# Optimization experiments

Hardware: AMD Instinct MI355X
Metric: run time of the kernel (lower is better)

The kernel has to match this reference:

```python
import jax, jax.numpy as jnp
import numpy as np

N = 50000
IN_CH = 64
HID_CH = 32
NEG_SLOPE = 0.2  # PyG GATConv default for attention LeakyReLU


def _glorot(key, shape):
    fan = shape[0] + shape[-1] if len(shape) > 1 else shape[0]
    s = jnp.sqrt(6.0 / fan)
    return jax.random.uniform(key, shape, jnp.float32, -s, s)


def setup_inputs() -> dict:
    key = jax.random.key(0)
    ks = jax.random.split(key, 20)
    x = jax.random.normal(ks[0], (N, IN_CH), jnp.float32)
    edge_index = jax.random.randint(ks[1], (2, 800000), 0, N, jnp.int64)
    dims = [(IN_CH, IN_CH), (IN_CH, HID_CH), (HID_CH, IN_CH), (IN_CH, IN_CH)]
    inp = {"x": x, "edge_index": edge_index}
    for i, (di, do) in enumerate(dims, 1):
        inp[f"w{i}"] = _glorot(ks[4 * i - 2], (di, do))
        inp[f"as{i}"] = _glorot(ks[4 * i - 1], (do,))
        inp[f"ad{i}"] = _glorot(ks[4 * i], (do,))
        inp[f"b{i}"] = jnp.zeros((do,), jnp.float32)
    return inp


def _gat_layer(x, src, dst, W, a_src, a_dst, b):
    # x: [N, di] -> h: [N, do]
    h = x @ W
    # per-edge attention logits (source + destination contributions)
    e = jax.nn.leaky_relu(h[src] @ a_src + h[dst] @ a_dst, NEG_SLOPE)  # [E]
    # numerically stable segment softmax over incoming edges per dst node
    m = jax.ops.segment_max(e, dst, num_segments=N)
    ex = jnp.exp(e - m[dst])
    denom = jax.ops.segment_sum(ex, dst, num_segments=N)
    alpha = ex / (denom[dst] + 1e-16)  # [E]
    out = jax.ops.segment_sum(alpha[:, None] * h[src], dst, num_segments=N)
    return out + b


def reference(x, edge_index, w1, as1, ad1, b1, w2, as2, ad2, b2,
              w3, as3, ad3, b3, w4, as4, ad4, b4):
    # PyG GATConv adds self-loops by default
    ar = jnp.arange(N, dtype=edge_index.dtype)
    src = jnp.concatenate([edge_index[0], ar])
    dst = jnp.concatenate([edge_index[1], ar])

    h1 = jax.nn.relu(_gat_layer(x, src, dst, w1, as1, ad1, b1))
    h = _gat_layer(h1, src, dst, w2, as2, ad2, b2)
    h3 = jax.nn.relu(h)
    h4 = jax.nn.relu(_gat_layer(h3, src, dst, w3, as3, ad3, b3))
    out = _gat_layer(h4, src, dst, w4, as4, ad4, b4)
    return (out, h)
```

## Files before the change

### kernel.cpp

```cpp
#include <hip/hip_runtime.h>
#include <hip/hip_fp16.h>
#include <math.h>

#define N_NODES 50000
#define N_EDGES 800000
#define E_TOT   850000
#define NEG_SLOPE 0.2f
#define NB_SCAN 49

typedef unsigned short u16;

__global__ void csr_init(int* deg) {
    int i = blockIdx.x * blockDim.x + threadIdx.x;
    if (i < N_NODES) deg[i] = 0;
}

__global__ void csr_degree(const int* __restrict__ dst, int* __restrict__ deg,
                           u16* __restrict__ rank) {
    int e = blockIdx.x * blockDim.x + threadIdx.x;
    if (e >= E_TOT) return;
    int d = (e < N_EDGES) ? dst[e] : (e - N_EDGES);
    rank[e] = (u16)atomicAdd(&deg[d], 1);
}

__global__ void scan_p1(const int* __restrict__ deg, int* __restrict__ bsum) {
    __shared__ int red[1024];
    int i = blockIdx.x * 1024 + threadIdx.x;
    red[threadIdx.x] = (i < N_NODES) ? deg[i] : 0;
    __syncthreads();
    for (int off = 512; off >= 1; off >>= 1) {
        if (threadIdx.x < off) red[threadIdx.x] += red[threadIdx.x + off];
        __syncthreads();
    }
    if (threadIdx.x == 0) bsum[blockIdx.x] = red[0];
}

__global__ void scan_p3(const int* __restrict__ deg, const int* __restrict__ bsum,
                        int* __restrict__ offs) {
    __shared__ int s[1024];
    __shared__ int bofs;
    int i = blockIdx.x * 1024 + threadIdx.x;
    int v = (i < N_NODES) ? deg[i] : 0;
    s[threadIdx.x] = v;
    if (threadIdx.x < 64) {
        int d = (threadIdx.x < NB_SCAN) ? bsum[threadIdx.x] : 0;
        int p = d;
        for (int off = 1; off < 64; off <<= 1) {
            int u = __shfl_up(p, off, 64);
            if ((int)threadIdx.x >= off) p += u;
        }
        if ((int)threadIdx.x == (int)blockIdx.x) bofs = p - d;
        if (blockIdx.x == NB_SCAN - 1 && threadIdx.x == NB_SCAN - 1)
            offs[N_NODES] = p;
    }
    __syncthreads();
    for (int off = 1; off < 1024; off <<= 1) {
        int u = (threadIdx.x >= off) ? s[threadIdx.x - off] : 0;
        __syncthreads();
        s[threadIdx.x] += u;
        __syncthreads();
    }
    if (i < N_NODES) offs[i] = bofs + s[threadIdx.x] - v;
}

__global__ void csr_fill(const int* __restrict__ src, const int* __restrict__ dst,
                         const u16* __restrict__ rank, const int* __restrict__ offs,
                         u16* __restrict__ csr_src) {
    int e = blockIdx.x * blockDim.x + threadIdx.x;
    if (e >= E_TOT) return;
    int s, d;
    if (e < N_EDGES) { s = src[e]; d = dst[e]; } else { s = e - N_EDGES; d = s; }
    csr_src[offs[d] + rank[e]] = (u16)s;
}

template<int DI, int DO>
__global__ void gemm_proj(const float* __restrict__ X, const float* __restrict__ W,
                          const float* __restrict__ a_src, const float* __restrict__ a_dst,
                          __half* __restrict__ Hh, float* __restrict__ ssrc,
                          float* __restrict__ sdst) {
    const int TPN = DO / 4;
    const int NPB = 256 / TPN;
    __shared__ float sW[DI * DO];
    __shared__ float sX[NPB][DI + 1];
    const int tid = threadIdx.x;
    for (int i = tid; i < DI * DO / 4; i += 256)
        ((float4*)sW)[i] = ((const float4*)W)[i];
    const int base = blockIdx.x * NPB;
    for (int i = tid; i < NPB * DI; i += 256) {
        int r = i / DI, col = i % DI;
        int node = base + r;
        sX[r][col] = (node < N_NODES) ? X[(long)node * DI + col] : 0.0f;
    }
    __syncthreads();
    const int cq = tid % TPN;
    const int g  = tid / TPN;
    const int node = base + g;
    if (node >= N_NODES) return;
    float ax = 0.0f, ay = 0.0f, az = 0.0f, aw = 0.0f;
    const float4* sW4 = (const float4*)sW;
#pragma unroll
    for (int k = 0; k < DI; k++) {
        float xv = sX[g][k];
        float4 w4 = sW4[k * TPN + cq];
        ax = fmaf(xv, w4.x, ax); ay = fmaf(xv, w4.y, ay);
        az = fmaf(xv, w4.z, az); aw = fmaf(xv, w4.w, aw);
    }
    union { uint2 u; __half2 h2[2]; } pk;
    pk.h2[0] = __float22half2_rn(make_float2(ax, ay));
    pk.h2[1] = __float22half2_rn(make_float2(az, aw));
    ((uint2*)(Hh + (long)node * DO))[cq] = pk.u;

    float4 as4 = ((const float4*)a_src)[cq];
    float4 ad4 = ((const float4*)a_dst)[cq];
    float ps = ax * as4.x + ay * as4.y + az * as4.z + aw * as4.w;
    float pd = ax * ad4.x + ay * ad4.y + az * ad4.z + aw * ad4.w;
#pragma unroll
    for (int m = TPN / 2; m >= 1; m >>= 1) {
        ps += __shfl_xor(ps, m, TPN);
        pd += __shfl_xor(pd, m, TPN);
    }
    if (cq == 0) { ssrc[node] = ps; sdst[node] = pd; }
}

template<int DIN, int DOUT>
__global__ void gather_gemm(const __half* __restrict__ Hh_in,
                            const float* __restrict__ ssrc_in,
                            const float* __restrict__ sdst_in,
                            const int* __restrict__ offs,
                            const u16* __restrict__ csr_src,
                            const float* __restrict__ bias_in,
                            int relu_o, float* __restrict__ extra_out,
                            const float* __restrict__ W2,
                            const float* __restrict__ a_src2,
                            const float* __restrict__ a_dst2,
                            __half* __restrict__ Hh_out,
                            float* __restrict__ ssrc2, float* __restrict__ sdst2) {
    const int G = DIN / 4;
    const int NPB = 256 / G;
    constexpr int LDSW = (DOUT > 0) ? DIN * DOUT : 1;
    __shared__ float sW[LDSW];
    if constexpr (DOUT > 0) {
        for (int i = threadIdx.x; i < DIN * DOUT / 4; i += 256)
            ((float4*)sW)[i] = ((const float4*)W2)[i];
        __syncthreads();
    }
    const int t = threadIdx.x;
    const int node = blockIdx.x * NPB + t / G;
    const int r = t % G;
    const bool valid = (node < N_NODES);
    const int beg = valid ? offs[node] : 0;
    const int end = valid ? offs[node + 1] : 0;
    const int deg = end - beg;
    const float sdv = valid ? sdst_in[node] : 0.0f;
    const uint2* H2 = (const uint2*)Hh_in;

    int   s0 = 0, s1 = 0;
    float ex0 = 0.0f, ex1 = 0.0f;
    if (r < deg)     s0 = csr_src[beg + r];
    if (G + r < deg) s1 = csr_src[beg + G + r];
    if (r < deg) {
        float v = ssrc_in[s0] + sdv;
        v = (v > 0.0f) ? v : NEG_SLOPE * v;
        ex0 = __expf(v);
    }
    if (G + r < deg) {
        float v = ssrc_in[s1] + sdv;
        v = (v > 0.0f) ? v : NEG_SLOPE * v;
        ex1 = __expf(v);
    }
    float den = ex0 + ex1;
    float4 acc = make_float4(0.0f, 0.0f, 0.0f, 0.0f);

#pragma unroll
    for (int j = 0; j < G; j++) {
        int   sa = __shfl(s0, j, G);
        float ea = __shfl(ex0, j, G);
        union { uint2 u; __half2 h2[2]; } ua;
        ua.u = H2[(long)sa * G + r];
        float2 a0 = __half22float2(ua.h2[0]), a1 = __half22float2(ua.h2[1]);
        acc.x = fmaf(ea, a0.x, acc.x); acc.y = fmaf(ea, a0.y, acc.y);
        acc.z = fmaf(ea, a1.x, acc.z); acc.w = fmaf(ea, a1.y, acc.w);
    }
    if (deg > G) {
#pragma unroll
        for (int j = 0; j < G; j++) {
            int   sa = __shfl(s1, j, G);
            float ea = __shfl(ex1, j, G);
            union { uint2 u; __half2 h2[2]; } ua;
            ua.u = H2[(long)sa * G + r];
            float2 a0 = __half22float2(ua.h2[0]), a1 = __half22float2(ua.h2[1]);
            acc.x = fmaf(ea, a0.x, acc.x); acc.y = fmaf(ea, a0.y, acc.y);
            acc.z = fmaf(ea, a1.x, acc.z); acc.w = fmaf(ea, a1.y, acc.w);
        }
    }
    for (int cb = beg + 2 * G; cb < end; cb += G) {
        int cnt = min(G, end - cb);
        int s2 = 0; float ex2 = 0.0f;
        if (r < cnt) {
            s2 = csr_src[cb + r];
            float v = ssrc_in[s2] + sdv;
            v = (v > 0.0f) ? v : NEG_SLOPE * v;
            ex2 = __expf(v);
        }
        den += ex2;
#pragma unroll
        for (int j = 0; j < G; j++) {
            int   sa = __shfl(s2, j, G);
            float ea = __shfl(ex2, j, G);
            union { uint2 u; __half2 h2[2]; } ua;
            ua.u = H2[(long)sa * G + r];
            float2 a0 = __half22float2(ua.h2[0]), a1 = __half22float2(ua.h2[1]);
            acc.x = fmaf(ea, a0.x, acc.x); acc.y = fmaf(ea, a0.y, acc.y);
            acc.z = fmaf(ea, a1.x, acc.z); acc.w = fmaf(ea, a1.y, acc.w);
        }
    }
#pragma unroll
    for (int m = G / 2; m >= 1; m >>= 1) den += __shfl_xor(den, m, G);

    float inv = 1.0f / (den + 1e-16f);
    float4 b4 = ((const float4*)bias_in)[r];
    float4 o;
    o.x = acc.x * inv + b4.x; o.y = acc.y * inv + b4.y;
    o.z = acc.z * inv + b4.z; o.w = acc.w * inv + b4.w;
    if (valid && extra_out) ((float4*)extra_out)[(long)node * G + r] = o;
    if (relu_o) {
        o.x = fmaxf(o.x, 0.0f); o.y = fmaxf(o.y, 0.0f);
        o.z = fmaxf(o.z, 0.0f); o.w = fmaxf(o.w, 0.0f);
    }

    if constexpr (DOUT > 0) {
        constexpr int C = DOUT / (DIN / 4);
        float acc2[C];
#pragma unroll
        for (int c = 0; c < C; c++) acc2[c] = 0.0f;
        const int cbase = r * C;
#pragma unroll
        for (int kb = 0; kb < G; kb++) {
            float4 o4;
            o4.x = __shfl(o.x, kb, G);
            o4.y = __shfl(o.y, kb, G);
            o4.z = __shfl(o.z, kb, G);
            o4.w = __shfl(o.w, kb, G);
            const float* wr = &sW[(4 * kb) * DOUT + cbase];
#pragma unroll
            for (int c = 0; c < C; c++) acc2[c] = fmaf(o4.x, wr[c], acc2[c]);
            wr += DOUT;
#pragma unroll
            for (int c = 0; c < C; c++) acc2[c] = fmaf(o4.y, wr[c], acc2[c]);
            wr += DOUT;
#pragma unroll
            for (int c = 0; c < C; c++) acc2[c] = fmaf(o4.z, wr[c], acc2[c]);
            wr += DOUT;
#pragma unroll
            for (int c = 0; c < C; c++) acc2[c] = fmaf(o4.w, wr[c], acc2[c]);
        }
        float ps = 0.0f, pd = 0.0f;
#pragma unroll
        for (int c = 0; c < C; c++) {
            ps = fmaf(acc2[c], a_src2[cbase + c], ps);
            pd = fmaf(acc2[c], a_dst2[cbase + c], pd);
        }
#pragma unroll
        for (int m = G / 2; m >= 1; m >>= 1) {
            ps += __shfl_xor(ps, m, G);
            pd += __shfl_xor(pd, m, G);
        }
        if (valid) {
            union { unsigned int u1; uint2 u2; uint4 u4; __half2 h[C / 2]; } pk;
#pragma unroll
            for (int c = 0; c < C; c += 2)
                pk.h[c / 2] = __float22half2_rn(make_float2(acc2[c], acc2[c + 1]));
            char* dp = (char*)(Hh_out + (long)node * DOUT + cbase);
            if constexpr (C == 2) *(unsigned int*)dp = pk.u1;
            else if constexpr (C == 4) *(uint2*)dp = pk.u2;
            else                        *(uint4*)dp = pk.u4;
            if (r == 0) { ssrc2[node] = ps; sdst2[node] = pd; }
        }
    }
}

extern "C" void kernel_launch(void* const* d_in, const int* in_sizes, int n_in,
                              void* d_out, int out_size, void* d_ws, size_t ws_size,
                              hipStream_t stream) {
    const float* x  = (const float*)d_in[0];
    const int*   ei = (const int*)d_in[1];

    const float* w1  = (const float*)d_in[2];
    const float* as1 = (const float*)d_in[3];
    const float* ad1 = (const float*)d_in[4];
    const float* b1  = (const float*)d_in[5];
    const float* w2  = (const float*)d_in[6];
    const float* as2 = (const float*)d_in[7];
    const float* ad2 = (const float*)d_in[8];
    const float* b2  = (const float*)d_in[9];
    const float* w3  = (const float*)d_in[10];
    const float* as3 = (const float*)d_in[11];
    const float* ad3 = (const float*)d_in[12];
    const float* b3  = (const float*)d_in[13];
    const float* w4  = (const float*)d_in[14];
    const float* as4 = (const float*)d_in[15];
    const float* ad4 = (const float*)d_in[16];
    const float* b4  = (const float*)d_in[17];

    float* out_final = (float*)d_out;
    float* out_h     = (float*)d_out + N_NODES * 64;

    float* ws    = (float*)d_ws;
    __half* Hh_a = (__half*)ws;
    __half* Hh_b = (__half*)(ws + N_NODES * 32);
    float* SS_a  = ws + 2 * N_NODES * 32;
    float* SD_a  = SS_a + N_NODES;
    float* SS_b  = SD_a + N_NODES;
    float* SD_b  = SS_b + N_NODES;
    int* deg     = (int*)(SD_b + N_NODES);
    u16* rank    = (u16*)(deg + N_NODES);
    int* offs    = (int*)(rank + E_TOT);
    u16* csr_src = (u16*)(offs + N_NODES + 1);
    int* bsum    = (int*)(csr_src + E_TOT);

    const int* src = ei;
    const int* dst = ei + N_EDGES;

    csr_init<<<(N_NODES + 255) / 256, 256, 0, stream>>>(deg);
    csr_degree<<<(E_TOT + 255) / 256, 256, 0, stream>>>(dst, deg, rank);
    scan_p1<<<NB_SCAN, 1024, 0, stream>>>(deg, bsum);
    scan_p3<<<NB_SCAN, 1024, 0, stream>>>(deg, bsum, offs);
    csr_fill<<<(E_TOT + 255) / 256, 256, 0, stream>>>(src, dst, rank, offs, csr_src);

    gemm_proj<64, 64><<<(N_NODES + 15) / 16, 256, 0, stream>>>(
        x, w1, as1, ad1, Hh_a, SS_a, SD_a);

    gather_gemm<64, 32><<<(N_NODES * 16 + 255) / 256, 256, 0, stream>>>(
        Hh_a, SS_a, SD_a, offs, csr_src, b1, 1, nullptr,
        w2, as2, ad2, Hh_b, SS_b, SD_b);
    gather_gemm<32, 64><<<(N_NODES * 8 + 255) / 256, 256, 0, stream>>>(
        Hh_b, SS_b, SD_b, offs, csr_src, b2, 1, out_h,
        w3, as3, ad3, Hh_a, SS_a, SD_a);
    gather_gemm<64, 64><<<(N_NODES * 16 + 255) / 256, 256, 0, stream>>>(
        Hh_a, SS_a, SD_a, offs, csr_src, b3, 1, nullptr,
        w4, as4, ad4, Hh_b, SS_b, SD_b);
    gather_gemm<64, 0><<<(N_NODES * 16 + 255) / 256, 256, 0, stream>>>(
        Hh_b, SS_b, SD_b, offs, csr_src, b4, 0, out_final,
        nullptr, nullptr, nullptr, nullptr, nullptr, nullptr);
}
```

Measured before the change: 270.9 us.

## Split gather across half-groups with 16-byte loads and cross-half reduction

The neighbor gather in the fused GAT kernel now has each lane load 8 fp16 features (uint4) instead of 4, with the two halves of each node group processing alternating edges. The partial sums are then combined with a shfl_xor across halves, and the epilogue GEMM is restructured around 8-wide chunks. This halves the number of gather load instructions and doubles bytes per request in the memory-bound aggregation. In exchange it adds 8 extra shuffles for the reduction and uses more registers.

```diff
diff --git a/kernel.cpp b/kernel.cpp
--- a/kernel.cpp
+++ b/kernel.cpp
@@ -135,8 +135,9 @@
                             const float* __restrict__ a_dst2,
                             __half* __restrict__ Hh_out,
                             float* __restrict__ ssrc2, float* __restrict__ sdst2) {
-    const int G = DIN / 4;
-    const int NPB = 256 / G;
+    constexpr int G = DIN / 4;
+    constexpr int L = DIN / 8;
+    constexpr int NPB = 256 / G;
     constexpr int LDSW = (DOUT > 0) ? DIN * DOUT : 1;
     __shared__ float sW[LDSW];
     if constexpr (DOUT > 0) {
@@ -147,12 +148,14 @@
     const int t = threadIdx.x;
     const int node = blockIdx.x * NPB + t / G;
     const int r = t % G;
+    const int hr = r / L;
+    const int q  = r % L;
     const bool valid = (node < N_NODES);
     const int beg = valid ? offs[node] : 0;
     const int end = valid ? offs[node + 1] : 0;
     const int deg = end - beg;
     const float sdv = valid ? sdst_in[node] : 0.0f;
-    const uint2* H2 = (const uint2*)Hh_in;
+    const uint4* H4 = (const uint4*)Hh_in;
 
     int   s0 = 0, s1 = 0;
     float ex0 = 0.0f, ex1 = 0.0f;
@@ -169,28 +172,36 @@
         ex1 = __expf(v);
     }
     float den = ex0 + ex1;
-    float4 acc = make_float4(0.0f, 0.0f, 0.0f, 0.0f);
-
-#pragma unroll
-    for (int j = 0; j < G; j++) {
-        int   sa = __shfl(s0, j, G);
-        float ea = __shfl(ex0, j, G);
-        union { uint2 u; __half2 h2[2]; } ua;
-        ua.u = H2[(long)sa * G + r];
-        float2 a0 = __half22float2(ua.h2[0]), a1 = __half22float2(ua.h2[1]);
-        acc.x = fmaf(ea, a0.x, acc.x); acc.y = fmaf(ea, a0.y, acc.y);
-        acc.z = fmaf(ea, a1.x, acc.z); acc.w = fmaf(ea, a1.y, acc.w);
+    float acc8[8];
+#pragma unroll
+    for (int c = 0; c < 8; c++) acc8[c] = 0.0f;
+
+#pragma unroll
+    for (int j = 0; j < G / 2; j++) {
+        int   sa = __shfl(s0, 2 * j + hr, G);
+        float ea = __shfl(ex0, 2 * j + hr, G);
+        union { uint4 u; __half2 h2[4]; } ua;
+        ua.u = H4[(long)sa * L + q];
+        float2 f0 = __half22float2(ua.h2[0]), f1 = __half22float2(ua.h2[1]);
+        float2 f2 = __half22float2(ua.h2[2]), f3 = __half22float2(ua.h2[3]);
+        acc8[0] = fmaf(ea, f0.x, acc8[0]); acc8[1] = fmaf(ea, f0.y, acc8[1]);
+        acc8[2] = fmaf(ea, f1.x, acc8[2]); acc8[3] = fmaf(ea, f1.y, acc8[3]);
+        acc8[4] = fmaf(ea, f2.x, acc8[4]); acc8[5] = fmaf(ea, f2.y, acc8[5]);
+        acc8[6] = fmaf(ea, f3.x, acc8[6]); acc8[7] = fmaf(ea, f3.y, acc8[7]);
     }
     if (deg > G) {
 #pragma unroll
-        for (int j = 0; j < G; j++) {
-            int   sa = __shfl(s1, j, G);
-            float ea = __shfl(ex1, j, G);
-            union { uint2 u; __half2 h2[2]; } ua;
-            ua.u = H2[(long)sa * G + r];
-            float2 a0 = __half22float2(ua.h2[0]), a1 = __half22float2(ua.h2[1]);
-            acc.x = fmaf(ea, a0.x, acc.x); acc.y = fmaf(ea, a0.y, acc.y);
-            acc.z = fmaf(ea, a1.x, acc.z); acc.w = fmaf(ea, a1.y, acc.w);
+        for (int j = 0; j < G / 2; j++) {
+            int   sa = __shfl(s1, 2 * j + hr, G);
+            float ea = __shfl(ex1, 2 * j + hr, G);
+            union { uint4 u; __half2 h2[4]; } ua;
+            ua.u = H4[(long)sa * L + q];
+            float2 f0 = __half22float2(ua.h2[0]), f1 = __half22float2(ua.h2[1]);
+            float2 f2 = __half22float2(ua.h2[2]), f3 = __half22float2(ua.h2[3]);
+            acc8[0] = fmaf(ea, f0.x, acc8[0]); acc8[1] = fmaf(ea, f0.y, acc8[1]);
+            acc8[2] = fmaf(ea, f1.x, acc8[2]); acc8[3] = fmaf(ea, f1.y, acc8[3]);
+            acc8[4] = fmaf(ea, f2.x, acc8[4]); acc8[5] = fmaf(ea, f2.y, acc8[5]);
+            acc8[6] = fmaf(ea, f3.x, acc8[6]); acc8[7] = fmaf(ea, f3.y, acc8[7]);
         }
     }
     for (int cb = beg + 2 * G; cb < end; cb += G) {
@@ -204,55 +215,59 @@
         }
         den += ex2;
 #pragma unroll
-        for (int j = 0; j < G; j++) {
-            int   sa = __shfl(s2, j, G);
-            float ea = __shfl(ex2, j, G);
-            union { uint2 u; __half2 h2[2]; } ua;
-            ua.u = H2[(long)sa * G + r];
-            float2 a0 = __half22float2(ua.h2[0]), a1 = __half22float2(ua.h2[1]);
-            acc.x = fmaf(ea, a0.x, acc.x); acc.y = fmaf(ea, a0.y, acc.y);
-            acc.z = fmaf(ea, a1.x, acc.z); acc.w = fmaf(ea, a1.y, acc.w);
-        }
-    }
+        for (int j = 0; j < G / 2; j++) {
+            int   sa = __shfl(s2, 2 * j + hr, G);
+            float ea = __shfl(ex2, 2 * j + hr, G);
+            union { uint4 u; __half2 h2[4]; } ua;
+            ua.u = H4[(long)sa * L + q];
+            float2 f0 = __half22float2(ua.h2[0]), f1 = __half22float2(ua.h2[1]);
+            float2 f2 = __half22float2(ua.h2[2]), f3 = __half22float2(ua.h2[3]);
+            acc8[0] = fmaf(ea, f0.x, acc8[0]); acc8[1] = fmaf(ea, f0.y, acc8[1]);
+            acc8[2] = fmaf(ea, f1.x, acc8[2]); acc8[3] = fmaf(ea, f1.y, acc8[3]);
+            acc8[4] = fmaf(ea, f2.x, acc8[4]); acc8[5] = fmaf(ea, f2.y, acc8[5]);
+            acc8[6] = fmaf(ea, f3.x, acc8[6]); acc8[7] = fmaf(ea, f3.y, acc8[7]);
+        }
+    }
+#pragma unroll
+    for (int c = 0; c < 8; c++) acc8[c] += __shfl_xor(acc8[c], L, G);
 #pragma unroll
     for (int m = G / 2; m >= 1; m >>= 1) den += __shfl_xor(den, m, G);
 
     float inv = 1.0f / (den + 1e-16f);
-    float4 b4 = ((const float4*)bias_in)[r];
-    float4 o;
-    o.x = acc.x * inv + b4.x; o.y = acc.y * inv + b4.y;
-    o.z = acc.z * inv + b4.z; o.w = acc.w * inv + b4.w;
-    if (valid && extra_out) ((float4*)extra_out)[(long)node * G + r] = o;
+    const float4* b4p = (const float4*)bias_in;
+    float4 bq0 = b4p[2 * q], bq1 = b4p[2 * q + 1];
+    float o8[8];
+    o8[0] = acc8[0] * inv + bq0.x; o8[1] = acc8[1] * inv + bq0.y;
+    o8[2] = acc8[2] * inv + bq0.z; o8[3] = acc8[3] * inv + bq0.w;
+    o8[4] = acc8[4] * inv + bq1.x; o8[5] = acc8[5] * inv + bq1.y;
+    o8[6] = acc8[6] * inv + bq1.z; o8[7] = acc8[7] * inv + bq1.w;
+    if (valid && extra_out) {
+        float4 st = (hr == 0) ? make_float4(o8[0], o8[1], o8[2], o8[3])
+                              : make_float4(o8[4], o8[5], o8[6], o8[7]);
+        ((float4*)extra_out)[(long)node * (2 * L) + 2 * q + hr] = st;
+    }
     if (relu_o) {
-        o.x = fmaxf(o.x, 0.0f); o.y = fmaxf(o.y, 0.0f);
-        o.z = fmaxf(o.z, 0.0f); o.w = fmaxf(o.w, 0.0f);
+#pragma unroll
+        for (int c = 0; c < 8; c++) o8[c] = fmaxf(o8[c], 0.0f);
     }
 
     if constexpr (DOUT > 0) {
-        constexpr int C = DOUT / (DIN / 4);
+        constexpr int C = DOUT / G;
         float acc2[C];
 #pragma unroll
         for (int c = 0; c < C; c++) acc2[c] = 0.0f;
         const int cbase = r * C;
 #pragma unroll
-        for (int kb = 0; kb < G; kb++) {
-            float4 o4;
-            o4.x = __shfl(o.x, kb, G);
-            o4.y = __shfl(o.y, kb, G);
-            o4.z = __shfl(o.z, kb, G);
-            o4.w = __shfl(o.w, kb, G);
-            const float* wr = &sW[(4 * kb) * DOUT + cbase];
-#pragma unroll
-            for (int c = 0; c < C; c++) acc2[c] = fmaf(o4.x, wr[c], acc2[c]);
-            wr += DOUT;
-#pragma unroll
-            for (int c = 0; c < C; c++) acc2[c] = fmaf(o4.y, wr[c], acc2[c]);
-            wr += DOUT;
-#pragma unroll
-            for (int c = 0; c < C; c++) acc2[c] = fmaf(o4.z, wr[c], acc2[c]);
-            wr += DOUT;
-#pragma unroll
-            for (int c = 0; c < C; c++) acc2[c] = fmaf(o4.w, wr[c], acc2[c]);
+        for (int kb = 0; kb < L; kb++) {
+            float v[8];
+#pragma unroll
+            for (int c8 = 0; c8 < 8; c8++) v[c8] = __shfl(o8[c8], kb, G);
+#pragma unroll
+            for (int c8 = 0; c8 < 8; c8++) {
+                const float* wr = &sW[(8 * kb + c8) * DOUT + cbase];
+#pragma unroll
+                for (int c = 0; c < C; c++) acc2[c] = fmaf(v[c8], wr[c], acc2[c]);
+            }
         }
         float ps = 0.0f, pd = 0.0f;
 #pragma unroll
```

After: 266.9 us. About the same (-1.5%).
